# Performance work log

Hardware: AMD Instinct MI355X
Metric: run time of the kernel (lower is better)

Reference implementation:

```python
import jax, jax.numpy as jnp
import numpy as np


def setup_inputs() -> dict:
    key = jax.random.key(0)
    k1, k2, k3, k4 = jax.random.split(key, 4)
    B, T, M, Din, Dout = 32, 24, 512, 64, 64
    x = jax.random.normal(k1, (B, T, M, Din), dtype=jnp.float32)
    adj = jax.random.uniform(k2, (M, M), dtype=jnp.float32)
    adj = adj / jnp.sum(adj, axis=-1, keepdims=True)  # row-normalized adjacency
    route_weights = jax.random.normal(k3, (M, Din, Dout), dtype=jnp.float32) * 0.05
    route_bias = jax.random.normal(k4, (M, 1, Dout), dtype=jnp.float32) * 0.05
    return {"x": x, "adj": adj, "route_weights": route_weights, "route_bias": route_bias}


def reference(x, adj, route_weights, route_bias):
    B, T, M, _ = x.shape
    xf = x.reshape(B * T, M, -1)                      # [BT, M, Din]
    # shared adjacency applied across all B*T graphs: one contraction instead of
    # a broadcast bmm
    h = jnp.einsum('mn,bnd->bmd', adj, xf)            # [BT, M, Din]
    # per-node (per-route) weight transform + per-route bias
    h = jnp.einsum('bmd,mdl->bml', h, route_weights)  # [BT, M, Dout]
    h = h + route_bias[:, 0, :][None, :, :]           # bias per route m
    return h.reshape(B, T, M, -1)
```

## Files before the change

### kernel.cpp

```cpp
#include <hip/hip_runtime.h>
#include <stdint.h>

typedef short bf16x8 __attribute__((ext_vector_type(8)));
typedef unsigned short u16x8 __attribute__((ext_vector_type(8)));
typedef float f32x4 __attribute__((ext_vector_type(4)));
typedef float f32x8 __attribute__((ext_vector_type(8)));

constexpr int BT_TOT = 768;
constexpr int M_N    = 512;
constexpr int DD     = 64;
constexpr int WROW   = 72;

constexpr size_t ADJ_FRAG_B = (size_t)M_N * M_N * 2;
constexpr size_t XTF_B      = (size_t)BT_TOT * M_N * DD * 2;
constexpr size_t HWS_B      = (size_t)BT_TOT * M_N * DD * 2;

__device__ __forceinline__ unsigned short f2bf(float f) {
  unsigned u = __builtin_bit_cast(unsigned, f);
  u += 0x7fffu + ((u >> 16) & 1u);
  return (unsigned short)(u >> 16);
}
__device__ __forceinline__ unsigned pk2(float a, float b) {
  return (unsigned)f2bf(a) | ((unsigned)f2bf(b) << 16);
}
__device__ __forceinline__ void gload16(const unsigned short* g, char* l) {
  __builtin_amdgcn_global_load_lds(
      (const __attribute__((address_space(1))) unsigned int*)g,
      (__attribute__((address_space(3))) unsigned int*)l, 16, 0, 0);
}

__global__ __launch_bounds__(256)
void prep_adj_frag(const float* __restrict__ adjg, unsigned short* __restrict__ wsadj) {
  int t  = blockIdx.x * 256 + threadIdx.x;
  int m  = t >> 6, ko = t & 63;
  f32x8 a = *(const f32x8*)(adjg + (size_t)m * M_N + ko * 8);
  u16x8 r;
  #pragma unroll
  for (int j = 0; j < 8; ++j) r[j] = f2bf(a[j]);
  size_t g = (size_t)((m >> 4) * 16 + (ko >> 2)) * 64 + (ko & 3) * 16 + (m & 15);
  *(u16x8*)(wsadj + g * 8) = r;
}

__global__ __launch_bounds__(256)
void prep_x_fast(const float* __restrict__ xg, unsigned short* __restrict__ xtf) {
  const int wid = blockIdx.x;
  const int bt  = wid >> 2, q = wid & 3;
  const int tid = threadIdx.x, lane = tid & 63, w = tid >> 6;
  const int gg  = lane >> 4, c4 = lane & 15;

  const float* xb = xg + (size_t)bt * (M_N * DD);
  unsigned short* xo = xtf + (size_t)bt * 32768;

  #pragma unroll
  for (int cc = 0; cc < 2; ++cc) {
    const int c = q * 2 + cc;
    unsigned r0[4], r1[4];
    #pragma unroll
    for (int s2 = 0; s2 < 2; ++s2) {
      #pragma unroll
      for (int sp = 0; sp < 2; ++sp) {
        const int n = c*64 + w*16 + (s2*2 + sp)*4 + gg;
        f32x4 xv = *(const f32x4*)(xb + (size_t)n * DD + c4*4);
        unsigned u0 = pk2(xv.x, xv.y), u1 = pk2(xv.z, xv.w);
        unsigned t0 = __shfl_xor(u0, 32), t1 = __shfl_xor(u1, 32);
        unsigned v0 = (gg & 2) ? t1 : u0, v1 = (gg & 2) ? u1 : t0;
        unsigned s0 = __shfl_xor(v0, 16), s1 = __shfl_xor(v1, 16);
        unsigned F0 = (gg & 1) ? ((s0 >> 16) | (v0 & 0xFFFF0000u))
                               : ((v0 & 0xFFFFu) | (s0 << 16));
        unsigned F1 = (gg & 1) ? ((s1 >> 16) | (v1 & 0xFFFF0000u))
                               : ((v1 & 0xFFFFu) | (s1 << 16));
        if (s2 == 0) { r0[sp*2] = F0; r0[sp*2+1] = F1; }
        else         { r1[sp*2] = F0; r1[sp*2+1] = F1; }
      }
    }
    const int d = c4*4 + gg, dt = d >> 4, l15p = d & 15;
    #pragma unroll
    for (int h = 0; h < 2; ++h) {
      const int o  = w*2 + h;
      const int kl = c*2 + (o >> 2), ggp = o & 3;
      uint4 val;
      if (h == 0) { val.x=r0[0]; val.y=r0[1]; val.z=r0[2]; val.w=r0[3]; }
      else        { val.x=r1[0]; val.y=r1[1]; val.z=r1[2]; val.w=r1[3]; }
      *(uint4*)(xo + ((size_t)(kl*4 + dt)*64 + ggp*16 + l15p) * 8) = val;
    }
  }
}

__global__ __launch_bounds__(256, 3)
void gconv_r13(const unsigned short* __restrict__ adjF,
               const unsigned short* __restrict__ xtf,
               unsigned short* __restrict__ h2) {
  __shared__ __align__(16) char lds[36864];

  const int wid  = blockIdx.x;
  const int xcd  = wid & 7, slot = wid >> 3;
  const int mb   = slot & 3;
  const int bt0  = ((slot >> 2) * 8 + xcd) * 2;

  const int tid  = threadIdx.x, lane = tid & 63, wv = tid >> 6;
  const int l15  = lane & 15, gg = lane >> 4;

  auto stage = [&](int c) {
    char* buf = lds + (c & 1) * 16384;
    #pragma unroll
    for (int j = 0; j < 4; ++j) {
      const int su = j*4 + wv;
      const int bb = su >> 3, kk = (su >> 2) & 1, dt = su & 3;
      const unsigned short* src = xtf + (size_t)(bt0 + bb) * 32768
                                + ((size_t)((2*c + kk)*4 + dt)*64 + lane) * 8;
      gload16(src, buf + su*1024 + lane*16);
    }
  };

  f32x4 acc[2][2][4];
  #pragma unroll
  for (int bb = 0; bb < 2; ++bb)
    #pragma unroll
    for (int mt = 0; mt < 2; ++mt)
      #pragma unroll
      for (int dt = 0; dt < 4; ++dt) acc[bb][mt][dt] = f32x4{0.f,0.f,0.f,0.f};

  stage(0);
  __syncthreads();

  #pragma unroll 1
  for (int c = 0; c < 8; ++c) {
    bf16x8 afr[2][2];
    #pragma unroll
    for (int kk = 0; kk < 2; ++kk)
      #pragma unroll
      for (int mt = 0; mt < 2; ++mt)
        afr[kk][mt] = __builtin_bit_cast(bf16x8, *(const u16x8*)(adjF
            + ((size_t)((mb*8 + wv*2 + mt)*16 + (2*c + kk))*64 + lane) * 8));
    if (c < 7) stage(c + 1);

    const char* buf = lds + (c & 1) * 16384;
    #pragma unroll
    for (int kk = 0; kk < 2; ++kk) {
      bf16x8 bfx[2][4];
      #pragma unroll
      for (int bb = 0; bb < 2; ++bb)
        #pragma unroll
        for (int dt = 0; dt < 4; ++dt)
          bfx[bb][dt] = __builtin_bit_cast(bf16x8,
              *(const u16x8*)(buf + ((bb*2 + kk)*4 + dt)*1024 + lane*16));
      #pragma unroll
      for (int bb = 0; bb < 2; ++bb)
        #pragma unroll
        for (int mt = 0; mt < 2; ++mt)
          #pragma unroll
          for (int dt = 0; dt < 4; ++dt)
            acc[bb][mt][dt] = __builtin_amdgcn_mfma_f32_16x16x32_bf16(
                afr[kk][mt], bfx[bb][dt], acc[bb][mt][dt], 0,0,0);
    }
    __syncthreads();
  }

  unsigned short* hl = (unsigned short*)lds;
  #pragma unroll
  for (int bb = 0; bb < 2; ++bb)
    #pragma unroll
    for (int mt = 0; mt < 2; ++mt)
      #pragma unroll
      for (int dt = 0; dt < 4; ++dt)
        #pragma unroll
        for (int r = 0; r < 4; ++r) {
          const int rl = bb*128 + wv*32 + mt*16 + gg*4 + r;
          hl[rl*72 + dt*16 + l15] = f2bf(acc[bb][mt][dt][r]);
        }
  __syncthreads();
  #pragma unroll
  for (int i = 0; i < 8; ++i) {
    const int g  = tid + i*256;
    const int rl = g >> 3, qq = g & 7;
    u16x8 v = *(const u16x8*)(hl + rl*72 + qq*8);
    const int bb = rl >> 7, mloc = rl & 127;
    const int m  = mb*128 + mloc, ks = qq >> 2, o = qq & 3;
    *(u16x8*)((char*)h2 + (((size_t)m*2 + ks)*768 + bt0 + bb)*64 + o*16) = v;
  }
}


__global__ __launch_bounds__(256)
void prep_adj(const float* __restrict__ adjg, unsigned short* __restrict__ wsadj) {
  int i = (blockIdx.x * 256 + threadIdx.x) * 8;
  f32x8 a = *(const f32x8*)(adjg + i);
  u16x8 r;
  #pragma unroll
  for (int j = 0; j < 8; ++j) r[j] = f2bf(a[j]);
  *(u16x8*)(wsadj + i) = r;
}

__global__ __launch_bounds__(256, 4)
void prep_x_fb(const float* __restrict__ xg, char* __restrict__ xout) {
  __shared__ __align__(16) char lds[2][8192];
  const int wid  = blockIdx.x;
  const int bt   = wid >> 1, half = wid & 1;
  const int tid  = threadIdx.x, lane = tid & 63, wv = tid >> 6;
  const int gg   = lane >> 4, c4 = lane & 15;
  const float* xb = xg + (size_t)bt * (M_N * DD);
  f32x4 xv[4];
  auto load_c = [&](int c) {
    #pragma unroll
    for (int s = 0; s < 4; ++s)
      xv[s] = *(const f32x4*)(xb + (size_t)(c*64 + s*16 + wv*4 + gg) * DD + c4*4);
  };
  load_c(half*4);
  #pragma unroll
  for (int cc = 0; cc < 4; ++cc) {
    const int c = half*4 + cc;
    char* xt = &lds[cc & 1][0];
    { const int d = c4*4 + gg, g3d = (d & 7) ^ ((d >> 3) & 7);
      #pragma unroll
      for (int s = 0; s < 4; ++s) {
        const int n4 = s*4 + wv;
        unsigned u0 = pk2(xv[s].x, xv[s].y), u1 = pk2(xv[s].z, xv[s].w);
        unsigned t0 = __shfl_xor(u0, 32), t1 = __shfl_xor(u1, 32);
        unsigned v0 = (gg & 2) ? t1 : u0, v1 = (gg & 2) ? u1 : t0;
        unsigned s0 = __shfl_xor(v0, 16), s1 = __shfl_xor(v1, 16);
        unsigned F0 = (gg & 1) ? ((s0 >> 16) | (v0 & 0xFFFF0000u))
                               : ((v0 & 0xFFFFu) | (s0 << 16));
        unsigned F1 = (gg & 1) ? ((s1 >> 16) | (v1 & 0xFFFF0000u))
                               : ((v1 & 0xFFFFu) | (s1 << 16));
        uint2 o2; o2.x = F0; o2.y = F1;
        *(uint2*)(xt + d*128 + (((n4 >> 1) ^ g3d) * 16) + (n4 & 1)*8) = o2;
      }
    }
    if (cc < 3) load_c(c + 1);
    __syncthreads();
    #pragma unroll
    for (int h = 0; h < 2; ++h) {
      const int g = tid + h*256, d = g >> 3, o = g & 7;
      const int g3d = (d & 7) ^ ((d >> 3) & 7);
      u16x8 val = *(const u16x8*)(xt + d*128 + ((o ^ g3d) * 16));
      *(u16x8*)(xout + ((size_t)(bt*512 + 8*d + c)) * 256 + 128 + o*16) = val;
    }
  }
}

template<bool WS>
__global__ __launch_bounds__(256, 3)
void gconv_fb(const float* __restrict__ adjf,
              const unsigned short* __restrict__ adjb,
              char* __restrict__ dio) {
  const int wid  = blockIdx.x;
  const int xcd  = wid & 7, slot = wid >> 3;
  const int mb   = slot & 3;
  const int bt0  = ((slot >> 2) * 8 + xcd) * 2;
  const int tid  = threadIdx.x, lane = tid & 63, wv = tid >> 6;
  const int l15  = lane & 15, gg = lane >> 4;
  const int mrow = mb*128 + wv*32;
  f32x4 acc[2][2][4];
  #pragma unroll
  for (int bb = 0; bb < 2; ++bb)
    #pragma unroll
    for (int mt = 0; mt < 2; ++mt)
      #pragma unroll
      for (int dt = 0; dt < 4; ++dt) acc[bb][mt][dt] = f32x4{0.f,0.f,0.f,0.f};
  #pragma unroll 4
  for (int kl = 0; kl < 16; ++kl) {
    bf16x8 afr[2];
    #pragma unroll
    for (int mt = 0; mt < 2; ++mt) {
      const int m = mrow + mt*16 + l15;
      if (WS) {
        afr[mt] = __builtin_bit_cast(bf16x8,
            *(const u16x8*)(adjb + (size_t)m*M_N + kl*32 + gg*8));
      } else {
        f32x8 a = *(const f32x8*)(adjf + (size_t)m*M_N + kl*32 + gg*8);
        u16x8 r;
        #pragma unroll
        for (int j = 0; j < 8; ++j) r[j] = f2bf(a[j]);
        afr[mt] = __builtin_bit_cast(bf16x8, r);
      }
    }
    bf16x8 bfx[2][4];
    #pragma unroll
    for (int bb = 0; bb < 2; ++bb)
      #pragma unroll
      for (int dt = 0; dt < 4; ++dt) {
        const int d = dt*16 + l15;
        bfx[bb][dt] = __builtin_bit_cast(bf16x8, *(const u16x8*)(dio
            + ((size_t)((bt0+bb)*512 + 8*d + (kl >> 1))) * 256
            + 128 + (kl & 1)*64 + gg*16));
      }
    #pragma unroll
    for (int bb = 0; bb < 2; ++bb)
      #pragma unroll
      for (int mt = 0; mt < 2; ++mt)
        #pragma unroll
        for (int dt = 0; dt < 4; ++dt)
          acc[bb][mt][dt] = __builtin_amdgcn_mfma_f32_16x16x32_bf16(
              afr[mt], bfx[bb][dt], acc[bb][mt][dt], 0,0,0);
  }
  #pragma unroll
  for (int bb = 0; bb < 2; ++bb)
    #pragma unroll
    for (int mt = 0; mt < 2; ++mt)
      #pragma unroll
      for (int dt = 0; dt < 4; ++dt)
        #pragma unroll
        for (int r = 0; r < 4; ++r) {
          const int m = mrow + mt*16 + gg*4 + r, d = dt*16 + l15;
          *(unsigned short*)(dio + ((size_t)(bt0+bb)*M_N + m)*256 + 2*d)
              = f2bf(acc[bb][mt][dt][r]);
        }
}

template<bool H2L>
__global__ __launch_bounds__(256, 4)
void route_mm(const char* __restrict__ hin,
              const float* __restrict__ wgt,
              const float* __restrict__ bias,
              float* __restrict__ outg) {
  __shared__ unsigned short wb[128 * WROW];
  const int m0    = blockIdx.x * 2;
  const int btblk = blockIdx.y * 64;
  const int tid   = threadIdx.x, lane = tid & 63, wv = tid >> 6;
  const int l15   = lane & 15, gg = lane >> 4;
  const int dp    = tid & 31, lo = tid >> 5;
  { const float* q = wgt + ((size_t)m0*64 + dp*2)*64 + lo*8;
    f32x8 w0 = *(const f32x8*)q;          f32x8 w1 = *(const f32x8*)(q+64);
    f32x8 w2 = *(const f32x8*)(q+4096);   f32x8 w3 = *(const f32x8*)(q+4160);
    #pragma unroll
    for (int e = 0; e < 8; ++e) {
      int lrow = lo*8 + e;
      *(unsigned*)(wb + lrow*WROW + dp*2)        = pk2(w0[e], w1[e]);
      *(unsigned*)(wb + (64 + lrow)*WROW + dp*2) = pk2(w2[e], w3[e]);
    }
  }
  __syncthreads();
  const int btw0 = btblk + wv*16;
  #pragma unroll
  for (int mm = 0; mm < 2; ++mm) {
    const int m = m0 + mm;
    bf16x8 afr[2];
    #pragma unroll
    for (int ks = 0; ks < 2; ++ks) {
      const char* hp = H2L
        ? hin + (((size_t)m*2 + ks)*768 + btw0 + l15)*64 + gg*16
        : hin + ((size_t)(btw0 + l15)*M_N + m)*256 + ks*64 + gg*16;
      afr[ks] = __builtin_bit_cast(bf16x8, *(const u16x8*)hp);
    }
    f32x4 acc[4];
    #pragma unroll
    for (int lt = 0; lt < 4; ++lt) acc[lt] = f32x4{0.f,0.f,0.f,0.f};
    #pragma unroll
    for (int lt = 0; lt < 4; ++lt)
      #pragma unroll
      for (int ks = 0; ks < 2; ++ks) {
        bf16x8 bfr = __builtin_bit_cast(bf16x8,
            *(const u16x8*)(wb + (mm*64 + lt*16 + l15)*WROW + ks*32 + gg*8));
        acc[lt] = __builtin_amdgcn_mfma_f32_16x16x32_bf16(afr[ks], bfr, acc[lt], 0,0,0);
      }
    #pragma unroll
    for (int lt = 0; lt < 4; ++lt) {
      float bv = bias[m*64 + lt*16 + l15];
      #pragma unroll
      for (int r = 0; r < 4; ++r) {
        size_t row = (size_t)(btw0 + gg*4 + r)*M_N + m;
        outg[row*64 + lt*16 + l15] = acc[lt][r] + bv;
      }
    }
  }
}

extern "C" void kernel_launch(void* const* d_in, const int* in_sizes, int n_in,
                              void* d_out, int out_size, void* d_ws, size_t ws_size,
                              hipStream_t stream) {
  const float* xg   = (const float*)d_in[0];
  const float* adjg = (const float*)d_in[1];
  const float* wgt  = (const float*)d_in[2];
  const float* bg   = (const float*)d_in[3];

  if (ws_size >= ADJ_FRAG_B + XTF_B + HWS_B) {
    unsigned short* adjF = (unsigned short*)d_ws;
    unsigned short* xtf  = (unsigned short*)((char*)d_ws + ADJ_FRAG_B);
    unsigned short* h2   = (unsigned short*)((char*)d_ws + ADJ_FRAG_B + XTF_B);
    prep_adj_frag<<<dim3(128), dim3(256), 0, stream>>>(adjg, adjF);
    prep_x_fast<<<dim3(BT_TOT * 4), dim3(256), 0, stream>>>(xg, xtf);
    gconv_r13<<<dim3(1536), dim3(256), 0, stream>>>(adjF, xtf, h2);
    route_mm<true><<<dim3(M_N/2, BT_TOT/64), dim3(256), 0, stream>>>(
        (const char*)h2, wgt, bg, (float*)d_out);
  } else {
    prep_x_fb<<<dim3(BT_TOT * 2), dim3(256), 0, stream>>>(xg, (char*)d_out);
    if (ws_size >= ADJ_FRAG_B) {
      unsigned short* wsadj = (unsigned short*)d_ws;
      prep_adj<<<dim3(M_N * M_N / (256 * 8)), dim3(256), 0, stream>>>(adjg, wsadj);
      gconv_fb<true><<<dim3(1536), dim3(256), 0, stream>>>(adjg, wsadj, (char*)d_out);
    } else {
      gconv_fb<false><<<dim3(1536), dim3(256), 0, stream>>>(adjg, nullptr, (char*)d_out);
    }
    route_mm<false><<<dim3(M_N/2, BT_TOT/64), dim3(256), 0, stream>>>(
        (const char*)d_out, wgt, bg, (float*)d_out);
  }
}
```

Before: 101.9 us.

## Pre-pack route weights into MFMA fragment layout and retile route kernel

After: 105.8 us. +3.8%, slower.

```diff
diff --git a/kernel.cpp b/kernel.cpp
--- a/kernel.cpp
+++ b/kernel.cpp
@@ -14,6 +14,7 @@
 constexpr size_t ADJ_FRAG_B = (size_t)M_N * M_N * 2;
 constexpr size_t XTF_B      = (size_t)BT_TOT * M_N * DD * 2;
 constexpr size_t HWS_B      = (size_t)BT_TOT * M_N * DD * 2;
+constexpr size_t W2_B       = (size_t)M_N * DD * DD * 2;
 
 __device__ __forceinline__ unsigned short f2bf(float f) {
   unsigned u = __builtin_bit_cast(unsigned, f);
@@ -86,6 +87,48 @@
   }
 }
 
+__global__ __launch_bounds__(256)
+void prep_w_frag(const float* __restrict__ wgt, unsigned short* __restrict__ w2) {
+  const int m0  = blockIdx.x * 2;
+  const int tid = threadIdx.x, lane = tid & 63, w = tid >> 6;
+  const int gg  = lane >> 4, c4 = lane & 15;
+
+  #pragma unroll
+  for (int cc = 0; cc < 2; ++cc) {
+    const int m = m0 + cc;
+    const float* wb = wgt + (size_t)m * 4096;
+    unsigned r0[4], r1[4];
+    #pragma unroll
+    for (int s2 = 0; s2 < 2; ++s2) {
+      #pragma unroll
+      for (int sp = 0; sp < 2; ++sp) {
+        const int d = w*16 + (s2*2 + sp)*4 + gg;
+        f32x4 xv = *(const f32x4*)(wb + (size_t)d * 64 + c4*4);
+        unsigned u0 = pk2(xv.x, xv.y), u1 = pk2(xv.z, xv.w);
+        unsigned t0 = __shfl_xor(u0, 32), t1 = __shfl_xor(u1, 32);
+        unsigned v0 = (gg & 2) ? t1 : u0, v1 = (gg & 2) ? u1 : t0;
+        unsigned s0 = __shfl_xor(v0, 16), s1 = __shfl_xor(v1, 16);
+        unsigned F0 = (gg & 1) ? ((s0 >> 16) | (v0 & 0xFFFF0000u))
+                               : ((v0 & 0xFFFFu) | (s0 << 16));
+        unsigned F1 = (gg & 1) ? ((s1 >> 16) | (v1 & 0xFFFF0000u))
+                               : ((v1 & 0xFFFFu) | (s1 << 16));
+        if (s2 == 0) { r0[sp*2] = F0; r0[sp*2+1] = F1; }
+        else         { r1[sp*2] = F0; r1[sp*2+1] = F1; }
+      }
+    }
+    const int l = c4*4 + gg, lt = l >> 4, l15p = l & 15;
+    #pragma unroll
+    for (int h = 0; h < 2; ++h) {
+      const int o  = w*2 + h;
+      const int ks = o >> 2, ggp = o & 3;
+      uint4 val;
+      if (h == 0) { val.x=r0[0]; val.y=r0[1]; val.z=r0[2]; val.w=r0[3]; }
+      else        { val.x=r1[0]; val.y=r1[1]; val.z=r1[2]; val.w=r1[3]; }
+      *(uint4*)(w2 + (((size_t)(m*4 + lt)*2 + ks)*64 + ggp*16 + l15p) * 8) = val;
+    }
+  }
+}
+
 __global__ __launch_bounds__(256, 3)
 void gconv_r13(const unsigned short* __restrict__ adjF,
                const unsigned short* __restrict__ xtf,
@@ -177,6 +220,64 @@
     const int bb = rl >> 7, mloc = rl & 127;
     const int m  = mb*128 + mloc, ks = qq >> 2, o = qq & 3;
     *(u16x8*)((char*)h2 + (((size_t)m*2 + ks)*768 + bt0 + bb)*64 + o*16) = v;
+  }
+}
+
+__global__ __launch_bounds__(256, 4)
+void route_v14(const unsigned short* __restrict__ h2,
+               const unsigned short* __restrict__ w2,
+               const float* __restrict__ bias,
+               float* __restrict__ outg) {
+  const int wid = blockIdx.x;
+  const int mp  = wid & 255, btg = wid >> 8;
+  const int m0  = mp * 2;
+  const int tid = threadIdx.x, lane = tid & 63, wv = tid >> 6;
+  const int l15 = lane & 15, gg = lane >> 4;
+  const int bt0 = btg*128 + wv*32;
+
+  #pragma unroll
+  for (int mm = 0; mm < 2; ++mm) {
+    const int m = m0 + mm;
+    bf16x8 bfr[4][2];
+    #pragma unroll
+    for (int lt = 0; lt < 4; ++lt)
+      #pragma unroll
+      for (int ks = 0; ks < 2; ++ks)
+        bfr[lt][ks] = __builtin_bit_cast(bf16x8, *(const u16x8*)(w2
+            + (((size_t)(m*4 + lt)*2 + ks)*64 + lane) * 8));
+    bf16x8 afr[2][2];
+    #pragma unroll
+    for (int tt = 0; tt < 2; ++tt)
+      #pragma unroll
+      for (int ks = 0; ks < 2; ++ks)
+        afr[tt][ks] = __builtin_bit_cast(bf16x8, *(const u16x8*)((const char*)h2
+            + (((size_t)m*2 + ks)*768 + bt0 + tt*16 + l15)*64 + gg*16));
+
+    f32x4 acc[2][4];
+    #pragma unroll
+    for (int tt = 0; tt < 2; ++tt)
+      #pragma unroll
+      for (int lt = 0; lt < 4; ++lt) acc[tt][lt] = f32x4{0.f,0.f,0.f,0.f};
+    #pragma unroll
+    for (int tt = 0; tt < 2; ++tt)
+      #pragma unroll
+      for (int lt = 0; lt < 4; ++lt)
+        #pragma unroll
+        for (int ks = 0; ks < 2; ++ks)
+          acc[tt][lt] = __builtin_amdgcn_mfma_f32_16x16x32_bf16(
+              afr[tt][ks], bfr[lt][ks], acc[tt][lt], 0,0,0);
+
+    #pragma unroll
+    for (int lt = 0; lt < 4; ++lt) {
+      const float bv = bias[m*64 + lt*16 + l15];
+      #pragma unroll
+      for (int tt = 0; tt < 2; ++tt)
+        #pragma unroll
+        for (int r = 0; r < 4; ++r) {
+          const int bt = bt0 + tt*16 + gg*4 + r;
+          outg[((size_t)bt*M_N + m)*DD + lt*16 + l15] = acc[tt][lt][r] + bv;
+        }
+    }
   }
 }
 
@@ -307,9 +408,8 @@
         }
 }
 
-template<bool H2L>
 __global__ __launch_bounds__(256, 4)
-void route_mm(const char* __restrict__ hin,
+void route_fb(const char* __restrict__ hin,
               const float* __restrict__ wgt,
               const float* __restrict__ bias,
               float* __restrict__ outg) {
@@ -337,9 +437,7 @@
     bf16x8 afr[2];
     #pragma unroll
     for (int ks = 0; ks < 2; ++ks) {
-      const char* hp = H2L
-        ? hin + (((size_t)m*2 + ks)*768 + btw0 + l15)*64 + gg*16
-        : hin + ((size_t)(btw0 + l15)*M_N + m)*256 + ks*64 + gg*16;
+      const char* hp = hin + ((size_t)(btw0 + l15)*M_N + m)*256 + ks*64 + gg*16;
       afr[ks] = __builtin_bit_cast(bf16x8, *(const u16x8*)hp);
     }
     f32x4 acc[4];
@@ -373,15 +471,16 @@
   const float* wgt  = (const float*)d_in[2];
   const float* bg   = (const float*)d_in[3];
 
-  if (ws_size >= ADJ_FRAG_B + XTF_B + HWS_B) {
+  if (ws_size >= ADJ_FRAG_B + XTF_B + HWS_B + W2_B) {
     unsigned short* adjF = (unsigned short*)d_ws;
     unsigned short* xtf  = (unsigned short*)((char*)d_ws + ADJ_FRAG_B);
     unsigned short* h2   = (unsigned short*)((char*)d_ws + ADJ_FRAG_B + XTF_B);
+    unsigned short* w2   = (unsigned short*)((char*)d_ws + ADJ_FRAG_B + XTF_B + HWS_B);
     prep_adj_frag<<<dim3(128), dim3(256), 0, stream>>>(adjg, adjF);
+    prep_w_frag<<<dim3(M_N/2), dim3(256), 0, stream>>>(wgt, w2);
     prep_x_fast<<<dim3(BT_TOT * 4), dim3(256), 0, stream>>>(xg, xtf);
     gconv_r13<<<dim3(1536), dim3(256), 0, stream>>>(adjF, xtf, h2);
-    route_mm<true><<<dim3(M_N/2, BT_TOT/64), dim3(256), 0, stream>>>(
-        (const char*)h2, wgt, bg, (float*)d_out);
+    route_v14<<<dim3(1536), dim3(256), 0, stream>>>(h2, w2, bg, (float*)d_out);
   } else {
     prep_x_fb<<<dim3(BT_TOT * 2), dim3(256), 0, stream>>>(xg, (char*)d_out);
     if (ws_size >= ADJ_FRAG_B) {
@@ -391,7 +490,7 @@
     } else {
       gconv_fb<false><<<dim3(1536), dim3(256), 0, stream>>>(adjg, nullptr, (char*)d_out);
     }
-    route_mm<false><<<dim3(M_N/2, BT_TOT/64), dim3(256), 0, stream>>>(
+    route_fb<<<dim3(M_N/2, BT_TOT/64), dim3(256), 0, stream>>>(
         (const char*)d_out, wgt, bg, (float*)d_out);
   }
 }
```
